# Kernel tuning notes

Hardware: AMD Instinct MI355X
Metric: run time of the kernel (lower is better)

Reference implementation:

```python
import jax, jax.numpy as jnp
import numpy as np

N = 50000      # nodes
E = 1600000    # edges (avg degree 32)
C = 48         # num_classes
S = 10         # num_steps


def setup_inputs() -> dict:
    key = jax.random.key(0)
    k1, k2, k3, k4 = jax.random.split(key, 4)
    edge_index = jax.random.randint(k1, (2, E), 0, N)
    edge_attr = jax.random.uniform(k2, (E,), dtype=jnp.float32)  # positive edge weights
    target = jax.random.randint(k3, (N,), 0, C)
    bound = 1.0 / np.sqrt(S)  # uniform(size, weight) init from PyG
    weight = jax.random.uniform(k4, (C, S), minval=-bound, maxval=bound, dtype=jnp.float32)
    return {"edge_index": edge_index, "edge_attr": edge_attr, "target": target, "weight": weight}


def reference(edge_index, edge_attr, target, weight):
    """Adaptive-diffusion random walk: propagate one-hot class indicators
    through a row-normalized weighted transition matrix for S steps and
    combine step-wise landing distributions with learned weight[c, s]."""
    row, col = edge_index[0], edge_index[1]
    # Row-normalize edge weights -> random-walk transition probabilities
    deg = jax.ops.segment_sum(edge_attr, row, num_segments=N)          # [N]
    norm = edge_attr / jnp.clip(deg, 1e-12)[row]                        # [E]
    h0 = jax.nn.one_hot(target, C, dtype=weight.dtype)                  # [N, C]

    def step(h, w_s):
        # message = P^T-style aggregation: scatter src features to dst
        h_new = jax.ops.segment_sum(norm[:, None] * h[row], col, num_segments=N)  # [N, C]
        return h_new, h_new * w_s  # w_s: [C], per-class step coefficient

    _, contribs = jax.lax.scan(step, h0, weight.T)  # contribs: [S, N, C]
    return contribs.sum(0)                          # [N, C]
```

## Files before the change

kernel.cpp:

```cpp
#include <hip/hip_runtime.h>
#include <hip/hip_fp16.h>

#define NN 50000
#define NE 1600000
#define NC 48
#define NS 10
#define PAD 88
#define PADN 50176

#define NBUCK 392
#define NB2   784
#define CAP   4608
#define EPB   2048
#define EPT   2

typedef __attribute__((ext_vector_type(8))) _Float16 half8;

__global__ __launch_bounds__(1024) void bin_kernel(const int* __restrict__ row,
        const int* __restrict__ col, const float* __restrict__ attr,
        int* __restrict__ bcur, uint2* __restrict__ bin, unsigned int* __restrict__ rbin) {
    __shared__ int hcnt[NB2];
    __shared__ int hbase[NB2];
    __shared__ int lofs[NB2];
    __shared__ int sc[1024];
    __shared__ uint2 stageC[EPB];
    __shared__ unsigned int stageR[EPB];
    int tid = threadIdx.x;
    if (tid < NB2) hcnt[tid] = 0;
    __syncthreads();
    int base = blockIdx.x * EPB;
    int ntot = min(EPB, NE - base);
    unsigned int rec[EPT];
    int cv[EPT];
    #pragma unroll
    for (int k = 0; k < EPT; ++k) {
        int e = base + k * 1024 + tid;
        if (e < NE) {
            int r = row[e], c = col[e];
            unsigned int iq = (unsigned int)rintf(attr[e] * 65535.0f);
            rec[k] = (iq << 16) | (unsigned int)r;
            cv[k] = c;
            atomicAdd(&hcnt[c >> 7], 1);
            atomicAdd(&hcnt[NBUCK + (r >> 7)], 1);
        } else {
            cv[k] = -1;
        }
    }
    __syncthreads();
    if (tid < NB2) hbase[tid] = atomicAdd(&bcur[tid], hcnt[tid]);
    sc[tid] = (tid < NB2) ? hcnt[tid] : 0;
    __syncthreads();
    for (int off = 1; off < 1024; off <<= 1) {
        int t = (tid >= off) ? sc[tid - off] : 0;
        __syncthreads();
        sc[tid] += t;
        __syncthreads();
    }
    if (tid < NB2) {
        lofs[tid] = sc[tid] - hcnt[tid];
        hcnt[tid] = 0;
    }
    __syncthreads();
    #pragma unroll
    for (int k = 0; k < EPT; ++k) {
        if (cv[k] >= 0) {
            int b = cv[k] >> 7;
            int rk = atomicAdd(&hcnt[b], 1);
            stageC[lofs[b] + rk] = make_uint2(rec[k], (unsigned int)cv[k]);
            int b2 = NBUCK + ((rec[k] & 0xffffu) >> 7);
            int rk2 = atomicAdd(&hcnt[b2], 1);
            stageR[lofs[b2] + rk2 - ntot] = rec[k];
        }
    }
    __syncthreads();
    for (int i = tid; i < ntot; i += 1024) {
        uint2 rc = stageC[i];
        int b = (int)(rc.y >> 7);
        bin[(size_t)b * CAP + hbase[b] + (i - lofs[b])] = rc;
    }
    for (int i = tid; i < ntot; i += 1024) {
        unsigned int rr = stageR[i];
        int b2 = NBUCK + ((rr & 0xffffu) >> 7);
        rbin[(size_t)(b2 - NBUCK) * CAP + hbase[b2] + (i + ntot - lofs[b2])] = rr;
    }
}

__global__ __launch_bounds__(1024) void place_deg_kernel(const int* __restrict__ bcur,
        const uint2* __restrict__ bin, const unsigned int* __restrict__ rbin,
        const int* __restrict__ target, unsigned int* __restrict__ edges,
        int* __restrict__ cnt, float* __restrict__ rdeg, int2* __restrict__ tq) {
    __shared__ int ccnt[128];
    __shared__ unsigned int acc[128];
    int b = blockIdx.x;
    if (threadIdx.x < 128) { ccnt[threadIdx.x] = 0; acc[threadIdx.x] = 0; }
    __syncthreads();
    int n2 = bcur[NBUCK + b];
    const unsigned int* rp2 = rbin + (size_t)b * CAP;
    for (int i = threadIdx.x; i < n2; i += 1024) {
        unsigned int rr = rp2[i];
        atomicAdd(&acc[rr & 127], rr >> 16);
    }
    int n = bcur[b];
    const uint2* rp = bin + (size_t)b * CAP;
    for (int i = threadIdx.x; i < n; i += 1024) {
        uint2 r = rp[i];
        int c = (int)r.y;
        int pos = atomicAdd(&ccnt[c & 127], 1);
        edges[(size_t)c * PAD + pos] = r.x;
    }
    __syncthreads();
    if (threadIdx.x < 128) {
        int v = (b << 7) + threadIdx.x;
        if (v < NN) {
            cnt[v] = ccnt[threadIdx.x];
            float rd = 65535.0f / fmaxf((float)acc[threadIdx.x], 1.0f);
            rdeg[v] = rd;
            tq[v] = make_int2(target[v], __float_as_int(rd));
        }
    }
}

__device__ __forceinline__ const half8* prow(unsigned int w_, const char* pb) {
    return reinterpret_cast<const half8*>(pb + (w_ & 0xffffu) * (NC * 2));
}

__device__ __forceinline__ void fma8(float* a, float wv, half8 g) {
    #pragma unroll
    for (int j = 0; j < 8; ++j) a[j] += wv * (float)g[j];
}


__global__ __launch_bounds__(256) void step1_kernel(const int* __restrict__ cnt,
        const unsigned int* __restrict__ edges, const int2* __restrict__ tq,
        const float* __restrict__ rdeg, _Float16* __restrict__ p_new) {
    int idx = blockIdx.x * blockDim.x + threadIdx.x;
    if (idx >= NN * 6) return;
    int v = idx / 6;
    int q = idx - v * 6;
    int n = cnt[v];
    const unsigned int* ep = edges + (size_t)v * PAD;
    int c0 = 8 * q;
    float a[8] = {0.f, 0.f, 0.f, 0.f, 0.f, 0.f, 0.f, 0.f};
    int i = 0;
    for (; i + 4 <= n; i += 4) {
        uint4 pa = *reinterpret_cast<const uint4*>(ep + i);
        int2 t0 = tq[pa.x & 0xffffu];
        int2 t1 = tq[pa.y & 0xffffu];
        int2 t2 = tq[pa.z & 0xffffu];
        int2 t3 = tq[pa.w & 0xffffu];
        float w0 = (float)(pa.x >> 16) * __int_as_float(t0.y);
        float w1 = (float)(pa.y >> 16) * __int_as_float(t1.y);
        float w2 = (float)(pa.z >> 16) * __int_as_float(t2.y);
        float w3 = (float)(pa.w >> 16) * __int_as_float(t3.y);
        int b0 = t0.x - c0, b1 = t1.x - c0, b2 = t2.x - c0, b3 = t3.x - c0;
        #pragma unroll
        for (int j = 0; j < 8; ++j) {
            a[j] += (b0 == j) ? w0 : 0.f;
            a[j] += (b1 == j) ? w1 : 0.f;
            a[j] += (b2 == j) ? w2 : 0.f;
            a[j] += (b3 == j) ? w3 : 0.f;
        }
    }
    for (; i < n; ++i) {
        unsigned int w_ = ep[i];
        int2 t0 = tq[w_ & 0xffffu];
        float w0 = (float)(w_ >> 16) * __int_as_float(t0.y);
        int b0 = t0.x - c0;
        #pragma unroll
        for (int j = 0; j < 8; ++j) a[j] += (b0 == j) ? w0 : 0.f;
    }
    float rd = rdeg[v] * (1.0f / 65535.0f);
    half8 ph;
    #pragma unroll
    for (int j = 0; j < 8; ++j) ph[j] = (_Float16)(a[j] * rd);
    __builtin_nontemporal_store(ph,
        reinterpret_cast<half8*>(p_new + (size_t)v * NC + c0));
}

__global__ __launch_bounds__(256) void gather_kernel(const int* __restrict__ cnt,
        const unsigned int* __restrict__ edges, const float* __restrict__ rdeg,
        const _Float16* __restrict__ p, _Float16* __restrict__ p_new) {
    int idx = blockIdx.x * blockDim.x + threadIdx.x;
    if (idx >= NN * 6) return;
    int v = idx / 6;
    int q = idx - v * 6;
    int n = cnt[v];
    const unsigned int* ep = edges + (size_t)v * PAD;
    const char* pb = (const char*)p + q * 16;
    float a[8] = {0.f, 0.f, 0.f, 0.f, 0.f, 0.f, 0.f, 0.f};
    const float sc = 1.0f / 65535.0f;
    int i = 0;
    for (; i + 8 <= n; i += 8) {
        uint4 pa = *reinterpret_cast<const uint4*>(ep + i);
        uint4 pc = *reinterpret_cast<const uint4*>(ep + i + 4);
        half8 g0 = *prow(pa.x, pb);
        half8 g1 = *prow(pa.y, pb);
        half8 g2 = *prow(pa.z, pb);
        half8 g3 = *prow(pa.w, pb);
        half8 g4 = *prow(pc.x, pb);
        half8 g5 = *prow(pc.y, pb);
        half8 g6 = *prow(pc.z, pb);
        half8 g7 = *prow(pc.w, pb);
        fma8(a, (float)(pa.x >> 16) * sc, g0);
        fma8(a, (float)(pa.y >> 16) * sc, g1);
        fma8(a, (float)(pa.z >> 16) * sc, g2);
        fma8(a, (float)(pa.w >> 16) * sc, g3);
        fma8(a, (float)(pc.x >> 16) * sc, g4);
        fma8(a, (float)(pc.y >> 16) * sc, g5);
        fma8(a, (float)(pc.z >> 16) * sc, g6);
        fma8(a, (float)(pc.w >> 16) * sc, g7);
    }
    if (i + 4 <= n) {
        uint4 pa = *reinterpret_cast<const uint4*>(ep + i);
        half8 g0 = *prow(pa.x, pb);
        half8 g1 = *prow(pa.y, pb);
        half8 g2 = *prow(pa.z, pb);
        half8 g3 = *prow(pa.w, pb);
        fma8(a, (float)(pa.x >> 16) * sc, g0);
        fma8(a, (float)(pa.y >> 16) * sc, g1);
        fma8(a, (float)(pa.z >> 16) * sc, g2);
        fma8(a, (float)(pa.w >> 16) * sc, g3);
        i += 4;
    }
    for (; i < n; ++i) {
        unsigned int w_ = ep[i];
        fma8(a, (float)(w_ >> 16) * sc, *prow(w_, pb));
    }

    float rd = rdeg[v];
    half8 ph;
    #pragma unroll
    for (int j = 0; j < 8; ++j) ph[j] = (_Float16)(a[j] * rd);
    __builtin_nontemporal_store(ph,
        reinterpret_cast<half8*>(p_new + (size_t)v * NC + q * 8));
}

__global__ __launch_bounds__(256) void finish_kernel(const float* __restrict__ rdeg,
        const _Float16* __restrict__ pS0, const float* __restrict__ weight,
        float* __restrict__ out) {
    int idx = blockIdx.x * blockDim.x + threadIdx.x;
    if (idx >= NN * 6) return;
    int v = idx / 6;
    int q = idx - v * 6;
    int c0 = 8 * q;
    size_t off = (size_t)v * NC + c0;
    float out8[8] = {0.f, 0.f, 0.f, 0.f, 0.f, 0.f, 0.f, 0.f};
    #pragma unroll
    for (int s = 0; s < NS; ++s) {
        half8 ph = *reinterpret_cast<const half8*>(pS0 + (size_t)s * (NN * NC) + off);
        #pragma unroll
        for (int j = 0; j < 8; ++j)
            out8[j] += (float)ph[j] * weight[(c0 + j) * NS + s];
    }
    float hinv = 1.0f / rdeg[v];
    *reinterpret_cast<float4*>(out + off) =
        make_float4(out8[0] * hinv, out8[1] * hinv, out8[2] * hinv, out8[3] * hinv);
    *reinterpret_cast<float4*>(out + off + 4) =
        make_float4(out8[4] * hinv, out8[5] * hinv, out8[6] * hinv, out8[7] * hinv);
}

extern "C" void kernel_launch(void* const* d_in, const int* in_sizes, int n_in,
                              void* d_out, int out_size, void* d_ws, size_t ws_size,
                              hipStream_t stream) {
    const int*   edge_index = (const int*)d_in[0];
    const float* edge_attr  = (const float*)d_in[1];
    const int*   target     = (const int*)d_in[2];
    const float* weight     = (const float*)d_in[3];
    float* out = (float*)d_out;

    const int* row = edge_index;
    const int* col = edge_index + NE;

    float*        rdeg  = (float*)d_ws;
    int*          bcur  = (int*)(rdeg + PADN);
    int*          cnt   = bcur + 1024;
    int2*         tq    = (int2*)(cnt + PADN);
    unsigned int* edges = (unsigned int*)(tq + NN);
    uint2*        bin   = (uint2*)(edges + (size_t)NN * PAD);
    _Float16*     pS0   = (_Float16*)(bin + (size_t)NBUCK * CAP);
    const size_t  PSTRIDE = (size_t)NN * NC;
    unsigned int* rbin  = (unsigned int*)(pS0 + (size_t)NS * PSTRIDE);

    (void)hipMemsetAsync(bcur, 0, 1024 * sizeof(int), stream);

    bin_kernel<<<(NE + EPB - 1) / EPB, 1024, 0, stream>>>(row, col, edge_attr,
            bcur, bin, rbin);
    place_deg_kernel<<<NBUCK, 1024, 0, stream>>>(bcur, bin, rbin, target,
            edges, cnt, rdeg, tq);

    const int gblocks = (NN * 6 + 255) / 256;
    step1_kernel<<<gblocks, 256, 0, stream>>>(cnt, edges, tq, rdeg, pS0);
    for (int t = 2; t <= NS; ++t) {
        gather_kernel<<<gblocks, 256, 0, stream>>>(cnt, edges, rdeg,
                pS0 + (size_t)(t - 2) * PSTRIDE, pS0 + (size_t)(t - 1) * PSTRIDE);
    }
    finish_kernel<<<gblocks, 256, 0, stream>>>(rdeg, pS0, weight, out);
}
```

Baseline: 357.4 us.

## Split feature buffer into per-quarter planar slabs and remap blocks to XCDs

Stores the fp16 propagation state as six class-chunk planes of [node][8] halfs instead of interleaved [node][48]. Each gather block now handles a single chunk, so the random 16-byte row reads for one chunk hit a compact 800KB slab instead of striding over the full 4.8MB array. Block indices are permuted so that consecutive blocks on the same XCD (blockIdx & 7) work on the same chunk plane, which should improve per-XCD L2 locality. Edge lists are now reread six times by separate blocks rather than by adjacent threads, which costs extra traffic, and stores are no longer nontemporal.

Measured after the change: 666.0 us. 1.86x slower.

```diff
diff --git a/kernel.cpp b/kernel.cpp
--- a/kernel.cpp
+++ b/kernel.cpp
@@ -13,6 +13,9 @@
 #define CAP   4608
 #define EPB   2048
 #define EPT   2
+
+#define QBLK  196
+#define GGRID (6*QBLK)
 
 typedef __attribute__((ext_vector_type(8))) _Float16 half8;
 
@@ -120,23 +123,22 @@
     }
 }
 
-__device__ __forceinline__ const half8* prow(unsigned int w_, const char* pb) {
-    return reinterpret_cast<const half8*>(pb + (w_ & 0xffffu) * (NC * 2));
+__device__ __forceinline__ const half8* prow16(unsigned int w_, const char* pb) {
+    return reinterpret_cast<const half8*>(pb + (w_ & 0xffffu) * 16);
 }
 
 __device__ __forceinline__ void fma8(float* a, float wv, half8 g) {
     #pragma unroll
     for (int j = 0; j < 8; ++j) a[j] += wv * (float)g[j];
 }
-
 
 __global__ __launch_bounds__(256) void step1_kernel(const int* __restrict__ cnt,
         const unsigned int* __restrict__ edges, const int2* __restrict__ tq,
         const float* __restrict__ rdeg, _Float16* __restrict__ p_new) {
-    int idx = blockIdx.x * blockDim.x + threadIdx.x;
-    if (idx >= NN * 6) return;
-    int v = idx / 6;
-    int q = idx - v * 6;
+    int lb = ((blockIdx.x & 7) * (GGRID / 8)) + (blockIdx.x >> 3);
+    int q = lb / QBLK;
+    int v = (lb - q * QBLK) * 256 + threadIdx.x;
+    if (v >= NN) return;
     int n = cnt[v];
     const unsigned int* ep = edges + (size_t)v * PAD;
     int c0 = 8 * q;
@@ -173,34 +175,33 @@
     half8 ph;
     #pragma unroll
     for (int j = 0; j < 8; ++j) ph[j] = (_Float16)(a[j] * rd);
-    __builtin_nontemporal_store(ph,
-        reinterpret_cast<half8*>(p_new + (size_t)v * NC + c0));
+    *reinterpret_cast<half8*>(p_new + ((size_t)q * PADN + v) * 8) = ph;
 }
 
 __global__ __launch_bounds__(256) void gather_kernel(const int* __restrict__ cnt,
         const unsigned int* __restrict__ edges, const float* __restrict__ rdeg,
         const _Float16* __restrict__ p, _Float16* __restrict__ p_new) {
-    int idx = blockIdx.x * blockDim.x + threadIdx.x;
-    if (idx >= NN * 6) return;
-    int v = idx / 6;
-    int q = idx - v * 6;
+    int lb = ((blockIdx.x & 7) * (GGRID / 8)) + (blockIdx.x >> 3);
+    int q = lb / QBLK;
+    int v = (lb - q * QBLK) * 256 + threadIdx.x;
+    if (v >= NN) return;
     int n = cnt[v];
     const unsigned int* ep = edges + (size_t)v * PAD;
-    const char* pb = (const char*)p + q * 16;
+    const char* pb = (const char*)(p + (size_t)q * PADN * 8);
     float a[8] = {0.f, 0.f, 0.f, 0.f, 0.f, 0.f, 0.f, 0.f};
     const float sc = 1.0f / 65535.0f;
     int i = 0;
     for (; i + 8 <= n; i += 8) {
         uint4 pa = *reinterpret_cast<const uint4*>(ep + i);
         uint4 pc = *reinterpret_cast<const uint4*>(ep + i + 4);
-        half8 g0 = *prow(pa.x, pb);
-        half8 g1 = *prow(pa.y, pb);
-        half8 g2 = *prow(pa.z, pb);
-        half8 g3 = *prow(pa.w, pb);
-        half8 g4 = *prow(pc.x, pb);
-        half8 g5 = *prow(pc.y, pb);
-        half8 g6 = *prow(pc.z, pb);
-        half8 g7 = *prow(pc.w, pb);
+        half8 g0 = *prow16(pa.x, pb);
+        half8 g1 = *prow16(pa.y, pb);
+        half8 g2 = *prow16(pa.z, pb);
+        half8 g3 = *prow16(pa.w, pb);
+        half8 g4 = *prow16(pc.x, pb);
+        half8 g5 = *prow16(pc.y, pb);
+        half8 g6 = *prow16(pc.z, pb);
+        half8 g7 = *prow16(pc.w, pb);
         fma8(a, (float)(pa.x >> 16) * sc, g0);
         fma8(a, (float)(pa.y >> 16) * sc, g1);
         fma8(a, (float)(pa.z >> 16) * sc, g2);
@@ -212,10 +213,10 @@
     }
     if (i + 4 <= n) {
         uint4 pa = *reinterpret_cast<const uint4*>(ep + i);
-        half8 g0 = *prow(pa.x, pb);
-        half8 g1 = *prow(pa.y, pb);
-        half8 g2 = *prow(pa.z, pb);
-        half8 g3 = *prow(pa.w, pb);
+        half8 g0 = *prow16(pa.x, pb);
+        half8 g1 = *prow16(pa.y, pb);
+        half8 g2 = *prow16(pa.z, pb);
+        half8 g3 = *prow16(pa.w, pb);
         fma8(a, (float)(pa.x >> 16) * sc, g0);
         fma8(a, (float)(pa.y >> 16) * sc, g1);
         fma8(a, (float)(pa.z >> 16) * sc, g2);
@@ -224,15 +225,14 @@
     }
     for (; i < n; ++i) {
         unsigned int w_ = ep[i];
-        fma8(a, (float)(w_ >> 16) * sc, *prow(w_, pb));
+        fma8(a, (float)(w_ >> 16) * sc, *prow16(w_, pb));
     }
 
     float rd = rdeg[v];
     half8 ph;
     #pragma unroll
     for (int j = 0; j < 8; ++j) ph[j] = (_Float16)(a[j] * rd);
-    __builtin_nontemporal_store(ph,
-        reinterpret_cast<half8*>(p_new + (size_t)v * NC + q * 8));
+    *reinterpret_cast<half8*>(p_new + ((size_t)q * PADN + v) * 8) = ph;
 }
 
 __global__ __launch_bounds__(256) void finish_kernel(const float* __restrict__ rdeg,
@@ -243,16 +243,17 @@
     int v = idx / 6;
     int q = idx - v * 6;
     int c0 = 8 * q;
-    size_t off = (size_t)v * NC + c0;
     float out8[8] = {0.f, 0.f, 0.f, 0.f, 0.f, 0.f, 0.f, 0.f};
     #pragma unroll
     for (int s = 0; s < NS; ++s) {
-        half8 ph = *reinterpret_cast<const half8*>(pS0 + (size_t)s * (NN * NC) + off);
+        half8 ph = *reinterpret_cast<const half8*>(
+            pS0 + ((size_t)(s * 6 + q) * PADN + v) * 8);
         #pragma unroll
         for (int j = 0; j < 8; ++j)
             out8[j] += (float)ph[j] * weight[(c0 + j) * NS + s];
     }
     float hinv = 1.0f / rdeg[v];
+    size_t off = (size_t)v * NC + c0;
     *reinterpret_cast<float4*>(out + off) =
         make_float4(out8[0] * hinv, out8[1] * hinv, out8[2] * hinv, out8[3] * hinv);
     *reinterpret_cast<float4*>(out + off + 4) =
@@ -278,7 +279,7 @@
     unsigned int* edges = (unsigned int*)(tq + NN);
     uint2*        bin   = (uint2*)(edges + (size_t)NN * PAD);
     _Float16*     pS0   = (_Float16*)(bin + (size_t)NBUCK * CAP);
-    const size_t  PSTRIDE = (size_t)NN * NC;
+    const size_t  PSTRIDE = (size_t)6 * PADN * 8;
     unsigned int* rbin  = (unsigned int*)(pS0 + (size_t)NS * PSTRIDE);
 
     (void)hipMemsetAsync(bcur, 0, 1024 * sizeof(int), stream);
@@ -288,11 +289,10 @@
     place_deg_kernel<<<NBUCK, 1024, 0, stream>>>(bcur, bin, rbin, target,
             edges, cnt, rdeg, tq);
 
-    const int gblocks = (NN * 6 + 255) / 256;
-    step1_kernel<<<gblocks, 256, 0, stream>>>(cnt, edges, tq, rdeg, pS0);
+    step1_kernel<<<GGRID, 256, 0, stream>>>(cnt, edges, tq, rdeg, pS0);
     for (int t = 2; t <= NS; ++t) {
-        gather_kernel<<<gblocks, 256, 0, stream>>>(cnt, edges, rdeg,
+        gather_kernel<<<GGRID, 256, 0, stream>>>(cnt, edges, rdeg,
                 pS0 + (size_t)(t - 2) * PSTRIDE, pS0 + (size_t)(t - 1) * PSTRIDE);
     }
-    finish_kernel<<<gblocks, 256, 0, stream>>>(rdeg, pS0, weight, out);
-}
+    finish_kernel<<<(NN * 6 + 255) / 256, 256, 0, stream>>>(rdeg, pS0, weight, out);
+}
```
